# Kernel tuning notes

Measured on AMD Instinct MI355X. Metric: run time of the kernel, lower is better.

The kernel has to match this reference:

```python
import jax, jax.numpy as jnp
import numpy as np
import math

N_STFT = 1025
N_MELS = 128
SAMPLE_RATE = 16000
F_MIN = 0.0
F_MAX = 8000.0
MAX_ITER = 20
LR = 0.3
MOMENTUM = 0.9
BATCH = 4
TIME = 1024


def _create_fb_matrix(n_freqs, f_min, f_max, n_mels, sample_rate):
    # Triangular mel filterbank, (n_freqs, n_mels), matching torchaudio's create_fb_matrix.
    all_freqs = np.linspace(0.0, sample_rate // 2, n_freqs)
    m_min = 2595.0 * math.log10(1.0 + f_min / 700.0)
    m_max = 2595.0 * math.log10(1.0 + f_max / 700.0)
    m_pts = np.linspace(m_min, m_max, n_mels + 2)
    f_pts = 700.0 * (10.0 ** (m_pts / 2595.0) - 1.0)
    f_diff = f_pts[1:] - f_pts[:-1]
    slopes = f_pts[None, :] - all_freqs[:, None]  # (n_freqs, n_mels+2)
    down_slopes = -slopes[:, :-2] / f_diff[:-1]
    up_slopes = slopes[:, 2:] / f_diff[1:]
    fb = np.maximum(0.0, np.minimum(down_slopes, up_slopes))
    return jnp.asarray(fb, dtype=jnp.float32)


def setup_inputs() -> dict:
    key = jax.random.key(0)
    k1, k2 = jax.random.split(key)
    melspec = jax.random.uniform(k1, (BATCH, N_MELS, TIME), dtype=jnp.float32)
    # torch.rand initialization of the estimated spectrogram, exposed for determinism
    spec_init = jax.random.uniform(k2, (BATCH, TIME, N_STFT), dtype=jnp.float32)
    fb = _create_fb_matrix(N_STFT, F_MIN, F_MAX, N_MELS, SAMPLE_RATE)
    return {"melspec": melspec, "spec_init": spec_init, "fb": fb}


def reference(melspec, spec_init, fb):
    # melspec: (B, n_mels, T) -> (B, T, n_mels); fb: (n_stft, n_mels)
    mel_t = jnp.swapaxes(melspec, -1, -2)
    b, t, _ = mel_t.shape
    inv = 2.0 / (b * t)  # d(mean over B*T of sum_m diff^2)/d(spec) prefactor

    def step(carry, _):
        spec, buf = carry
        diff = mel_t - jnp.einsum('btf,fm->btm', spec, fb)      # (B,T,M)
        grad = -inv * jnp.einsum('btm,fm->btf', diff, fb)       # (B,T,F)
        buf = MOMENTUM * buf + grad                              # SGD momentum buffer
        spec = jnp.maximum(spec - LR * buf, 0.0)                 # update + clamp(min=0)
        return (spec, buf), None

    init = (spec_init, jnp.zeros_like(spec_init))
    (spec, _), _ = jax.lax.scan(step, init, None, length=MAX_ITER)
    return jnp.swapaxes(spec, -1, -2)  # (B, n_stft, T)
```

## Files before the change

### kernel.cpp

```cpp
#include <hip/hip_runtime.h>
#include <math.h>
#include <stdint.h>

#define N_STFT 1025
#define N_MELS 128
#define BATCH 4
#define TIME 1024
#define MAX_ITER 20

typedef unsigned int u32;
typedef unsigned long long u64;

__global__ __launch_bounds__(256)
__attribute__((amdgpu_waves_per_eu(2, 4))) void imel_main(
    const float* __restrict__ melspec, const float* __restrict__ spec_init,
    const int* __restrict__ m0f, const float* __restrict__ w0a,
    const float* __restrict__ w1a, float* __restrict__ out) {
  __shared__ u32   s_P[4][N_MELS];
  __shared__ float s_mel[4][N_MELS];
  __shared__ float s_out[4][1060];

  const int tid = threadIdx.x;
  const int w   = tid >> 6;
  const int l   = tid & 63;
  const int flat = (blockIdx.x & 7) * 128 + (blockIdx.x >> 3);
  const int b   = flat >> 8;
  const int t0  = (flat & 255) << 2;
  const int tA  = t0 + w;

  for (int i = tid; i < 4 * N_MELS; i += 256) {
    const int m = i >> 2, r = i & 3;
    s_mel[r][m] = melspec[((size_t)b * N_MELS + m) * TIME + t0 + r];
  }
  __syncthreads();

  const float SCALE = 16777216.0f;
  const float SC48  = 281474976710656.0f;
  const float LRI48 = 5.2041704279304213e-19f;

  float rs[16], rb[16], rw0[16], rw1[16], cc[16];
  int rm[16];

  const float* srow = spec_init + (size_t)(b * TIME + tA) * N_STFT;
  const float* melW = &s_mel[w][0];
#pragma unroll
  for (int k = 0; k < 16; ++k) {
    const int f = (l << 4) + k;
    rs[k] = srow[f];
    const int m = m0f[f];
    rm[k] = m;
    const float w0 = w0a[f], w1 = w1a[f];
    rw0[k] = w0 * SCALE;
    rw1[k] = w1 * SCALE;
    cc[k] = -SC48 * fmaf(melW[m], w0, melW[m + 1] * w1);
    rb[k] = 0.f;
  }
  const float rt = (l == 63) ? srow[1024] : 0.f;

  bool adv[16];
  adv[0] = false;
#pragma unroll
  for (int k = 1; k < 16; ++k) adv[k] = (rm[k] != rm[k - 1]);

  u32* __restrict__ Pw = &s_P[w][0];
  ((u64*)Pw)[l] = 0ULL;

  {
    const int phase = ((blockIdx.x >> 3) + w) & 3;
    for (int i = 0; i < phase; ++i) __builtin_amdgcn_s_sleep(3);
  }

  for (int it = 0; it < MAX_ITER; ++it) {
    {
      float a0 = rs[0] * rw0[0], a1 = rs[0] * rw1[0];
#pragma unroll
      for (int k = 1; k < 16; ++k) {
        if (adv[k]) atomicAdd(&Pw[rm[k - 1]], (u32)(a0 + 0.5f));
        const float n0 = (adv[k] ? a1 : a0) + rs[k] * rw0[k];
        a1 = (adv[k] ? 0.f : a1) + rs[k] * rw1[k];
        a0 = n0;
      }
      atomicAdd(&Pw[rm[15]],     (u32)(a0 + 0.5f));
      atomicAdd(&Pw[rm[15] + 1], (u32)(a1 + 0.5f));
    }
    __builtin_amdgcn_wave_barrier();
#pragma unroll
    for (int k = 0; k < 16; ++k) {
      const float p0 = (float)(int)Pw[rm[k]];
      const float p1 = (float)(int)Pw[rm[k] + 1];
      const float g  = fmaf(p1, rw1[k], fmaf(p0, rw0[k], cc[k]));
      rb[k] = fmaf(0.9f, rb[k], g);
      rs[k] = fmaxf(fmaf(-LRI48, rb[k], rs[k]), 0.f);
    }
    __builtin_amdgcn_wave_barrier();
    ((u64*)Pw)[l] = 0ULL;
    __builtin_amdgcn_wave_barrier();
  }

#pragma unroll
  for (int k = 0; k < 16; ++k) {
    const int f = (l << 4) + k;
    s_out[w][f + (f >> 5)] = rs[k];
  }
  if (l == 63) s_out[w][1056] = rt;
  __syncthreads();

  const int tl = tid & 3;
  const int fg = tid >> 2;
  float* obase = out + (size_t)b * N_STFT * TIME + t0 + tl;
  for (int f = fg; f < N_STFT; f += 64) {
    obase[(size_t)f * TIME] = s_out[tl][f + (f >> 5)];
  }
}

static unsigned char g_tab[15360];
static bool g_tab_ready = false;

static float host_fbval(double freq, const double* f_pts, int m) {
  const double down = (freq - f_pts[m]) / (f_pts[m + 1] - f_pts[m]);
  const double up = (f_pts[m + 2] - freq) / (f_pts[m + 2] - f_pts[m + 1]);
  double v = down < up ? down : up;
  if (v < 0.0) v = 0.0;
  return (float)v;
}

static void build_tab() {
  double f_pts[130];
  const double m_max = 2595.0 * log10(1.0 + 8000.0 / 700.0);
  for (int i = 0; i < 130; ++i) {
    const double m = (double)i * m_max / 129.0;
    f_pts[i] = 700.0 * (pow(10.0, m / 2595.0) - 1.0);
  }
  int* m0f = (int*)g_tab;
  float* w0a = (float*)(g_tab + 5120);
  float* w1a = (float*)(g_tab + 10240);
  for (int f = 0; f < N_STFT; ++f) {
    const double freq = (double)f * (8000.0 / 1024.0);
    int m0 = 0;
    for (int m = 0; m < N_MELS; ++m) {
      if (host_fbval(freq, f_pts, m) != 0.0f) { m0 = m; break; }
    }
    if (m0 > N_MELS - 2) m0 = N_MELS - 2;
    m0f[f] = m0;
    w0a[f] = host_fbval(freq, f_pts, m0);
    w1a[f] = host_fbval(freq, f_pts, m0 + 1);
  }
}

extern "C" void kernel_launch(void* const* d_in, const int* in_sizes, int n_in,
                              void* d_out, int out_size, void* d_ws, size_t ws_size,
                              hipStream_t stream) {
  const float* melspec = (const float*)d_in[0];
  const float* spec_init = (const float*)d_in[1];
  float* out = (float*)d_out;

  if (!g_tab_ready) { build_tab(); g_tab_ready = true; }

  int* m0f = (int*)d_ws;
  float* w0a = (float*)((char*)d_ws + 5120);
  float* w1a = (float*)((char*)d_ws + 10240);

  hipMemcpyAsync(d_ws, g_tab, sizeof(g_tab), hipMemcpyHostToDevice, stream);
  imel_main<<<dim3(1024), dim3(256), 0, stream>>>(melspec, spec_init, m0f, w0a, w1a, out);
}
```

Before: 115.9 us.

## Fold mel target into LDS accumulator init and pack update math with pk_fma

Seeds each per-wave mel accumulator with the negated fixed-point mel target, so the subtraction happens inside the integer atomics and the per-bin cc register array goes away. The per-bin gradient, momentum and spec update now use packed v_pk_fma/v_pk_mul f32 instructions on pairs of bins. It also drops the staggered s_sleep phase offset and recomputes the segment-advance flags inline. The intent is fewer VALU instructions and less register pressure, at the cost of a different fixed-point rounding path and possible atomic contention once the start stagger is gone.

```diff
diff --git a/kernel.cpp b/kernel.cpp
--- a/kernel.cpp
+++ b/kernel.cpp
@@ -10,6 +10,18 @@
 
 typedef unsigned int u32;
 typedef unsigned long long u64;
+typedef float f32x2 __attribute__((ext_vector_type(2)));
+
+__device__ __forceinline__ f32x2 pk_fma(f32x2 a, f32x2 b, f32x2 c) {
+  f32x2 d;
+  asm("v_pk_fma_f32 %0, %1, %2, %3" : "=v"(d) : "v"(a), "v"(b), "v"(c));
+  return d;
+}
+__device__ __forceinline__ f32x2 pk_mul(f32x2 a, f32x2 b) {
+  f32x2 d;
+  asm("v_pk_mul_f32 %0, %1, %2" : "=v"(d) : "v"(a), "v"(b));
+  return d;
+}
 
 __global__ __launch_bounds__(256)
 __attribute__((amdgpu_waves_per_eu(2, 4))) void imel_main(
@@ -35,10 +47,10 @@
   __syncthreads();
 
   const float SCALE = 16777216.0f;
-  const float SC48  = 281474976710656.0f;
-  const float LRI48 = 5.2041704279304213e-19f;
+  const float INV48 = 3.5527136788005009e-15f;
+  const float LRI   = 0.3f * (2.0f / (BATCH * TIME));
 
-  float rs[16], rb[16], rw0[16], rw1[16], cc[16];
+  f32x2 rsp[8], rbp[8], rw0p[8], rw1p[8];
   int rm[16];
 
   const float* srow = spec_init + (size_t)(b * TIME + tA) * N_STFT;
@@ -46,61 +58,76 @@
 #pragma unroll
   for (int k = 0; k < 16; ++k) {
     const int f = (l << 4) + k;
-    rs[k] = srow[f];
-    const int m = m0f[f];
+    const float s  = srow[f];
+    const int   m  = m0f[f];
     rm[k] = m;
-    const float w0 = w0a[f], w1 = w1a[f];
-    rw0[k] = w0 * SCALE;
-    rw1[k] = w1 * SCALE;
-    cc[k] = -SC48 * fmaf(melW[m], w0, melW[m + 1] * w1);
-    rb[k] = 0.f;
+    const float w0 = w0a[f] * SCALE;
+    const float w1 = w1a[f] * SCALE;
+    if (k & 1) {
+      rsp[k >> 1].y = s;  rw0p[k >> 1].y = w0;
+      rw1p[k >> 1].y = w1; rbp[k >> 1].y = 0.f;
+    } else {
+      rsp[k >> 1].x = s;  rw0p[k >> 1].x = w0;
+      rw1p[k >> 1].x = w1; rbp[k >> 1].x = 0.f;
+    }
   }
   const float rt = (l == 63) ? srow[1024] : 0.f;
 
-  bool adv[16];
-  adv[0] = false;
-#pragma unroll
-  for (int k = 1; k < 16; ++k) adv[k] = (rm[k] != rm[k - 1]);
+  const int mi0 = __float2int_rn(melW[2 * l] * SCALE);
+  const int mi1 = __float2int_rn(melW[2 * l + 1] * SCALE);
+  const u64 pinit = (u64)(u32)(-mi0) | ((u64)(u32)(-mi1) << 32);
 
   u32* __restrict__ Pw = &s_P[w][0];
-  ((u64*)Pw)[l] = 0ULL;
+  ((u64*)Pw)[l] = pinit;
 
-  {
-    const int phase = ((blockIdx.x >> 3) + w) & 3;
-    for (int i = 0; i < phase; ++i) __builtin_amdgcn_s_sleep(3);
-  }
+#define RS_(k) ((k & 1) ? rsp[k >> 1].y : rsp[k >> 1].x)
+#define RW0_(k) ((k & 1) ? rw0p[k >> 1].y : rw0p[k >> 1].x)
+#define RW1_(k) ((k & 1) ? rw1p[k >> 1].y : rw1p[k >> 1].x)
+
+  const f32x2 PK_NINE = {0.9f, 0.9f};
+  const f32x2 PK_INV48 = {INV48, INV48};
+  const f32x2 PK_NLRI = {-LRI, -LRI};
 
   for (int it = 0; it < MAX_ITER; ++it) {
     {
-      float a0 = rs[0] * rw0[0], a1 = rs[0] * rw1[0];
+      float a0 = RS_(0) * RW0_(0), a1 = RS_(0) * RW1_(0);
 #pragma unroll
       for (int k = 1; k < 16; ++k) {
-        if (adv[k]) atomicAdd(&Pw[rm[k - 1]], (u32)(a0 + 0.5f));
-        const float n0 = (adv[k] ? a1 : a0) + rs[k] * rw0[k];
-        a1 = (adv[k] ? 0.f : a1) + rs[k] * rw1[k];
+        const bool adv = (rm[k] != rm[k - 1]);
+        if (adv) atomicAdd(&Pw[rm[k - 1]], (u32)__float2int_rn(a0));
+        const float n0 = (adv ? a1 : a0) + RS_(k) * RW0_(k);
+        a1 = (adv ? 0.f : a1) + RS_(k) * RW1_(k);
         a0 = n0;
       }
-      atomicAdd(&Pw[rm[15]],     (u32)(a0 + 0.5f));
-      atomicAdd(&Pw[rm[15] + 1], (u32)(a1 + 0.5f));
+      atomicAdd(&Pw[rm[15]],     (u32)__float2int_rn(a0));
+      atomicAdd(&Pw[rm[15] + 1], (u32)__float2int_rn(a1));
     }
     __builtin_amdgcn_wave_barrier();
 #pragma unroll
-    for (int k = 0; k < 16; ++k) {
-      const float p0 = (float)(int)Pw[rm[k]];
-      const float p1 = (float)(int)Pw[rm[k] + 1];
-      const float g  = fmaf(p1, rw1[k], fmaf(p0, rw0[k], cc[k]));
-      rb[k] = fmaf(0.9f, rb[k], g);
-      rs[k] = fmaxf(fmaf(-LRI48, rb[k], rs[k]), 0.f);
+    for (int j = 0; j < 8; ++j) {
+      const u32 qa0 = Pw[rm[2 * j]];
+      const u32 qa1 = Pw[rm[2 * j] + 1];
+      const u32 qb0 = Pw[rm[2 * j + 1]];
+      const u32 qb1 = Pw[rm[2 * j + 1] + 1];
+      f32x2 p0, p1;
+      p0.x = (float)(int)qa0; p0.y = (float)(int)qb0;
+      p1.x = (float)(int)qa1; p1.y = (float)(int)qb1;
+      const f32x2 t = pk_fma(p0, rw0p[j], pk_mul(p1, rw1p[j]));
+      const f32x2 g = pk_mul(t, PK_INV48);
+      rbp[j] = pk_fma(PK_NINE, rbp[j], g);
+      const f32x2 u = pk_fma(PK_NLRI, rbp[j], rsp[j]);
+      rsp[j].x = fmaxf(u.x, 0.f);
+      rsp[j].y = fmaxf(u.y, 0.f);
     }
     __builtin_amdgcn_wave_barrier();
-    ((u64*)Pw)[l] = 0ULL;
+    ((u64*)Pw)[l] = pinit;
     __builtin_amdgcn_wave_barrier();
   }
 
 #pragma unroll
   for (int k = 0; k < 16; ++k) {
     const int f = (l << 4) + k;
-    s_out[w][f + (f >> 5)] = rs[k];
+    s_out[w][f + (f >> 5)] = RS_(k);
   }
   if (l == 63) s_out[w][1056] = rt;
   __syncthreads();
```

New measurement: 118.0 us. About the same (+1.9%).
